# Performance work log

Hardware: AMD Instinct MI355X
Metric: run time of the kernel (lower is better)

Reference implementation:

```python
import jax, jax.numpy as jnp
import numpy as np
import math

NUM_HEADS = 16
HIDDEN = 1024
HEAD_DIM = HIDDEN // NUM_HEADS
MAX_POS = 512
BUCKET = 256
SCALE = 1.0 / math.sqrt(3.0 * HEAD_DIM)


def _make_log_bucket_position(rel_pos):
    # rel_pos: int32 [S, S]
    mid = BUCKET // 2
    rp = rel_pos.astype(jnp.float32)
    sign = jnp.sign(rp)
    abs_pos = jnp.where((rel_pos < mid) & (rel_pos > -mid), float(mid - 1), jnp.abs(rp))
    log_pos = jnp.ceil(jnp.log(abs_pos / mid) * (mid - 1) / math.log((MAX_POS - 1) / mid)) + mid
    bucket_pos = jnp.where(abs_pos <= mid, rp, log_pos * sign)
    return bucket_pos.astype(jnp.int32)


def _get_rel_pos(num_positions):
    ids = jnp.arange(num_positions, dtype=jnp.int32)
    rel_pos = ids[:, None] - ids[None, :]  # [S, S]
    return _make_log_bucket_position(rel_pos)


def setup_inputs() -> dict:
    key = jax.random.key(0)
    ks = jax.random.split(key, 10)
    B, S = 8, 512
    s_in = 1.0 / math.sqrt(HIDDEN)
    inputs = jax.random.normal(ks[0], (B, S, HIDDEN), dtype=jnp.float32)
    rel_embeddings = jax.random.normal(ks[1], (B, 2 * BUCKET, HIDDEN), dtype=jnp.float32)
    Wq = jax.random.normal(ks[2], (HIDDEN, NUM_HEADS, HEAD_DIM), dtype=jnp.float32) * s_in
    Wk = jax.random.normal(ks[3], (HIDDEN, NUM_HEADS, HEAD_DIM), dtype=jnp.float32) * s_in
    Wv = jax.random.normal(ks[4], (HIDDEN, NUM_HEADS, HEAD_DIM), dtype=jnp.float32) * s_in
    bq = jnp.zeros((NUM_HEADS, HEAD_DIM), dtype=jnp.float32)
    bk = jnp.zeros((NUM_HEADS, HEAD_DIM), dtype=jnp.float32)
    bv = jnp.zeros((NUM_HEADS, HEAD_DIM), dtype=jnp.float32)
    Wo = jax.random.normal(ks[5], (HIDDEN, HIDDEN), dtype=jnp.float32) * s_in
    bo = jnp.zeros((HIDDEN,), dtype=jnp.float32)
    return {"inputs": inputs, "rel_embeddings": rel_embeddings,
            "Wq": Wq, "bq": bq, "Wk": Wk, "bk": bk, "Wv": Wv, "bv": bv,
            "Wo": Wo, "bo": bo}


def reference(inputs, rel_embeddings, Wq, bq, Wk, bk, Wv, bv, Wo, bo):
    B, S, _ = inputs.shape
    # projections: [B,S,H,D]
    query = jnp.einsum('bsc,chd->bshd', inputs, Wq) + bq
    key = jnp.einsum('bsc,chd->bshd', inputs, Wk) + bk
    value = jnp.einsum('bsc,chd->bshd', inputs, Wv) + bv

    # content-content scores: [B,H,S_q,S_k]
    scores = jnp.einsum('bkhd,bqhd->bhqk', key, query) * SCALE

    # relative position projections on rel_embeddings [B,P,hidden], P=2*BUCKET
    pos_query = jnp.einsum('bpc,chd->bphd', rel_embeddings, Wq) + bq
    pos_key = jnp.einsum('bpc,chd->bphd', rel_embeddings, Wk) + bk

    rel_pos = _get_rel_pos(S)  # [S,S] int32
    span = BUCKET

    # c2p: query vs pos_key -> [B,H,S,P], gather along last axis
    c2p = jnp.einsum('bphd,bqhd->bhqp', pos_key, query)
    c2p_pos = jnp.clip(rel_pos + span, 0, 2 * span - 1)  # [S,S]
    c2p_idx = jnp.broadcast_to(c2p_pos[None, None], (B, NUM_HEADS, S, S))
    c2p = jnp.take_along_axis(c2p, c2p_idx, axis=3) * SCALE

    # p2c: key vs pos_query -> [B,H,S,P], gather then transpose
    p2c = jnp.einsum('bphd,bkhd->bhkp', pos_query, key)
    p2c_pos = jnp.clip(-rel_pos + span, 0, 2 * span - 1)
    p2c_idx = jnp.broadcast_to(p2c_pos[None, None], (B, NUM_HEADS, S, S))
    p2c = jnp.take_along_axis(p2c, p2c_idx, axis=3)
    p2c = jnp.swapaxes(p2c, 2, 3) * SCALE

    scores = scores + c2p + p2c
    probs = jax.nn.softmax(scores.astype(jnp.float32), axis=-1).astype(inputs.dtype)

    # attend: [B,S,H,D] -> [B,S,hidden]
    attn_out = jnp.einsum('bhqk,bkhd->bqhd', probs, value)
    attn_out = attn_out.reshape(B, S, HIDDEN)
    return jnp.einsum('bsc,cd->bsd', attn_out, Wo) + bo
```

## Files before the change

kernel.cpp:

```cpp
#include <hip/hip_runtime.h>

#define NUM_HEADS 16
#define HEAD_DIM  64
#define HIDDEN    1024
#define SEQ       512
#define BATCH     8
#define NBH       128
#define POSN      512
#define SCALE_F   0.07216878364870323f

typedef __attribute__((ext_vector_type(8))) short  short8;
typedef __attribute__((ext_vector_type(4))) short  short4_t;
typedef __attribute__((ext_vector_type(4))) float  floatx4;

#define GLDS16(gsrc, ldst) \
    __builtin_amdgcn_global_load_lds((const __attribute__((address_space(1))) void*)(gsrc), \
                                     (__attribute__((address_space(3))) void*)(ldst), 16, 0, 0)

__device__ __forceinline__ float bits2f(short s) {
    union { unsigned u; float f; } x;
    x.u = ((unsigned)(unsigned short)s) << 16;
    return x.f;
}
__device__ __forceinline__ short f2bits(float f) {
    union { float f; unsigned u; } x;
    x.f = f;
    unsigned r = x.u + 0x7fffu + ((x.u >> 16) & 1u);
    return (short)(r >> 16);
}

__global__ __launch_bounds__(256)
void prep_all(const float* __restrict__ a, const float* __restrict__ b,
              short* __restrict__ oa, short* __restrict__ ob,
              const float* __restrict__ w0, const float* __restrict__ w1,
              const float* __restrict__ w2, const float* __restrict__ w3,
              short* __restrict__ o0, short* __restrict__ o1,
              short* __restrict__ o2, short* __restrict__ o3,
              int* __restrict__ ftab)
{
    __shared__ float tile[64][65];
    const int bid = blockIdx.x, t = threadIdx.x;

    if (bid < 4096) {
        const int idx = bid * 256 + t;
        floatx4 va = ((const floatx4*)a)[idx];
        floatx4 vb = ((const floatx4*)b)[idx];
        short4_t ra, rb;
#pragma unroll
        for (int i = 0; i < 4; i++) { ra[i] = f2bits(va[i]); rb[i] = f2bits(vb[i]); }
        ((short4_t*)oa)[idx] = ra;
        ((short4_t*)ob)[idx] = rb;
        return;
    }
    if (bid < 5120) {
        const int r = bid - 4096;
        const int z = r >> 8, rem = r & 255;
        const float* src = (z == 0) ? w0 : (z == 1) ? w1 : (z == 2) ? w2 : w3;
        short*       dst = (z == 0) ? o0 : (z == 1) ? o1 : (z == 2) ? o2 : o3;
        const int c0 = (rem & 15) * 64, n0 = (rem >> 4) * 64;
#pragma unroll
        for (int j = 0; j < 16; j++) {
            const int e = t + j * 256;
            tile[e >> 6][e & 63] = src[(long)(c0 + (e >> 6)) * 1024 + n0 + (e & 63)];
        }
        __syncthreads();
#pragma unroll
        for (int j = 0; j < 16; j++) {
            const int e = t + j * 256;
            dst[(long)(n0 + (e >> 6)) * 1024 + c0 + (e & 63)] = f2bits(tile[e & 63][e >> 6]);
        }
        return;
    }
    const int i = (bid - 5120) * 256 + t;
    if (i >= 1023) return;
    const int delta = i - 511;
    const float Cf = (float)log(511.0 / 128.0);
    float absp = (delta < 128 && delta > -128) ? 127.0f : fabsf((float)delta);
    float bucket;
    if (absp <= 128.0f) {
        bucket = (float)delta;
    } else {
        float lp = ceilf((logf(absp * (1.0f / 128.0f)) * 127.0f) / Cf) + 128.0f;
        bucket = (delta > 0) ? lp : -lp;
    }
    int bi = (int)bucket + 256;
    bi = min(max(bi, 0), 511);
    ftab[i] = bi;
}

template<int MODE>
__global__ __launch_bounds__(256)
void gemm_nt(const short* __restrict__ A, long aBatch, int lda,
             const short* __restrict__ BT, long bBatch, int ldb,
             void* __restrict__ O0, void* __restrict__ O1, void* __restrict__ O2,
             long oBatch, int ldo,
             const float* __restrict__ b0, const float* __restrict__ b1,
             const float* __restrict__ b2, int Kd,
             const short* __restrict__ A2,
             void* __restrict__ O3, void* __restrict__ O4)
{
    __shared__ __align__(16) short As[2][128 * 64];
    __shared__ __align__(16) short Bs[2][128 * 64];

    int m0, n0, yy = 0;
    bool z1 = false;
    const int z = blockIdx.z;
    if (MODE == 6) {
        const int lin = blockIdx.x + (blockIdx.y << 5);
        const int swz = (lin & 7) * 160 + (lin >> 3);
        m0 = (swz & 31) * 128;
        yy = swz >> 5;
        z1 = (yy >= 24);
        n0 = (z1 ? (yy - 24) : yy) * 128;
    } else {
        m0 = blockIdx.x * 128;
        n0 = blockIdx.y * 128;
    }

    const short* Ab;
    const short* Bb;
    if (MODE == 6) {
        Ab = z1 ? A2 : A;
        Bb = BT;
    } else {
        Ab = A + (long)z * aBatch;
        Bb = BT + (long)z * bBatch;
    }

    const int t = threadIdx.x;
    const int l = t & 63, w = t >> 6;
    const int wm = w >> 1, wn = w & 1;
    const int lr = l & 15, lg = l >> 4;

    floatx4 acc[4][4];
#pragma unroll
    for (int i = 0; i < 4; i++)
#pragma unroll
        for (int j = 0; j < 4; j++) acc[i][j] = (floatx4){0.f, 0.f, 0.f, 0.f};

#pragma unroll
    for (int j = 0; j < 4; j++) {
        const int c = (w * 4 + j) * 64 + l;
        const int row = c >> 3, pc = c & 7;
        const int cc = pc ^ (row & 7);
        GLDS16(Ab + (long)(m0 + row) * lda + cc * 8, As[0] + c * 8);
        GLDS16(Bb + (long)(n0 + row) * ldb + cc * 8, Bs[0] + c * 8);
    }
    __syncthreads();

    int cur = 0;
    for (int k0 = 0; k0 < Kd; k0 += 64, cur ^= 1) {
        if (k0 + 64 < Kd) {
            const int kn = k0 + 64;
#pragma unroll
            for (int j = 0; j < 4; j++) {
                const int c = (w * 4 + j) * 64 + l;
                const int row = c >> 3, pc = c & 7;
                const int cc = pc ^ (row & 7);
                GLDS16(Ab + (long)(m0 + row) * lda + kn + cc * 8, As[cur ^ 1] + c * 8);
                GLDS16(Bb + (long)(n0 + row) * ldb + kn + cc * 8, Bs[cur ^ 1] + c * 8);
            }
        }
#pragma unroll
        for (int ks = 0; ks < 2; ks++) {
            short8 af[4], bfr[4];
#pragma unroll
            for (int i = 0; i < 4; i++) {
                const int mr = wm * 64 + i * 16 + lr;
                af[i] = *(const short8*)((char*)As[cur] + mr * 128 + (((ks * 4 + lg) ^ (mr & 7)) * 16));
                const int nr = wn * 64 + i * 16 + lr;
                bfr[i] = *(const short8*)((char*)Bs[cur] + nr * 128 + (((ks * 4 + lg) ^ (nr & 7)) * 16));
            }
#pragma unroll
            for (int i = 0; i < 4; i++)
#pragma unroll
                for (int j = 0; j < 4; j++)
                    acc[i][j] = __builtin_amdgcn_mfma_f32_16x16x32_bf16(af[i], bfr[j], acc[i][j], 0, 0, 0);
        }
        __syncthreads();
    }

    if (MODE == 6 && !z1 && yy >= 16) {
        short* tp = &As[0][0];
#pragma unroll
        for (int i = 0; i < 4; i++)
#pragma unroll
            for (int j = 0; j < 4; j++)
#pragma unroll
                for (int e = 0; e < 4; e++) {
                    const int ml  = wm * 64 + i * 16 + lg * 4 + e;
                    const int ngl = wn * 64 + j * 16 + lr;
                    const float v = acc[i][j][e] + b2[(n0 & 1023) + ngl];
                    tp[ngl * 128 + (ml ^ ((ngl & 7) << 4))] = f2bits(v);
                }
        __syncthreads();
        const int b = m0 >> 9, s0 = m0 & 511;
        const int hb = (n0 & 1023) >> 6;
        short* dst = (short*)O2;
#pragma unroll
        for (int j = 0; j < 8; j++) {
            const int task = t + j * 256;
            const int r = task >> 4, c = task & 15;
            short8 v8 = *(const short8*)(tp + r * 128 + ((c * 8) ^ ((r & 7) << 4)));
            const int h = hb + (r >> 6), d = r & 63;
            *(short8*)(dst + ((long)((b * NUM_HEADS + h) * HEAD_DIM + d)) * SEQ + s0 + c * 8) = v8;
        }
        return;
    }

#pragma unroll
    for (int i = 0; i < 4; i++) {
#pragma unroll
        for (int j = 0; j < 4; j++) {
#pragma unroll
            for (int e = 0; e < 4; e++) {
                const int mg = m0 + wm * 64 + i * 16 + lg * 4 + e;
                const int ng = n0 + wn * 64 + j * 16 + lr;
                float v = acc[i][j][e];
                if (MODE == 1) {
                    ((short*)O0)[(long)z * oBatch + (long)mg * ldo + ng] = f2bits(v);
                } else if (MODE == 2) {
                    ((float*)O0)[(long)mg * ldo + ng] = v + b0[ng];
                } else if (MODE == 6) {
                    const int hh = ng & 1023, mat = ng >> 10;
                    const int h = hh >> 6, d = hh & 63;
                    const int b = mg >> 9, s = mg & 511;
                    v += (mat == 0 ? b0 : b1)[hh];
                    short* dst;
                    if (z1) dst = (short*)(mat == 0 ? O3 : O4);
                    else    dst = (short*)(mat == 0 ? O0 : O1);
                    dst[((long)(b * NUM_HEADS + h) * SEQ + s) * HEAD_DIM + d] = f2bits(v);
                }
            }
        }
    }
}

template<int MODE>
__global__ __launch_bounds__(256)
void gemm_nt3(const short* __restrict__ A, long aBatch, int lda,
              const short* __restrict__ BT, long bBatch, int ldb,
              void* __restrict__ O0, long oBatch, int ldo,
              const float* __restrict__ b0, int Kd)
{
    __shared__ __align__(16) short LB[24576];

    const int z = blockIdx.z;
    const int m0 = blockIdx.x * 128, n0 = blockIdx.y * 128;
    const short* Ab = A + (long)z * aBatch;
    const short* Bb = BT + (long)z * bBatch;

    const int t = threadIdx.x;
    const int l = t & 63, w = t >> 6;
    const int wm = w >> 1, wn = w & 1;
    const int lr = l & 15, lg = l >> 4;

    const int c0c = t, c1c = t + 256;
    const int r0 = c0c >> 2, cc0 = (c0c & 3) ^ ((r0 >> 1) & 3);
    const int r1 = c1c >> 2, cc1 = (c1c & 3) ^ ((r1 >> 1) & 3);

    floatx4 acc[4][4];
#pragma unroll
    for (int i = 0; i < 4; i++)
#pragma unroll
        for (int j = 0; j < 4; j++) acc[i][j] = (floatx4){0.f, 0.f, 0.f, 0.f};

    const int niter = Kd >> 5;

    {
        GLDS16(Ab + (long)(m0 + r0) * lda + cc0 * 8, LB + c0c * 8);
        GLDS16(Ab + (long)(m0 + r1) * lda + cc1 * 8, LB + c1c * 8);
        GLDS16(Bb + (long)(n0 + r0) * ldb + cc0 * 8, LB + 12288 + c0c * 8);
        GLDS16(Bb + (long)(n0 + r1) * ldb + cc1 * 8, LB + 12288 + c1c * 8);
        GLDS16(Ab + (long)(m0 + r0) * lda + 32 + cc0 * 8, LB + 4096 + c0c * 8);
        GLDS16(Ab + (long)(m0 + r1) * lda + 32 + cc1 * 8, LB + 4096 + c1c * 8);
        GLDS16(Bb + (long)(n0 + r0) * ldb + 32 + cc0 * 8, LB + 12288 + 4096 + c0c * 8);
        GLDS16(Bb + (long)(n0 + r1) * ldb + 32 + cc1 * 8, LB + 12288 + 4096 + c1c * 8);
    }

    int cbase = 0;
    int ibase = 8192;
    for (int i = 0; i < niter; i++) {
        __builtin_amdgcn_sched_barrier(0);
        if (i + 1 < niter) { asm volatile("s_waitcnt vmcnt(4)" ::: "memory"); }
        else               { asm volatile("s_waitcnt vmcnt(0)" ::: "memory"); }
        __builtin_amdgcn_s_barrier();
        __builtin_amdgcn_sched_barrier(0);
        if (i + 2 < niter) {
            const int kn = (i + 2) << 5;
            GLDS16(Ab + (long)(m0 + r0) * lda + kn + cc0 * 8, LB + ibase + c0c * 8);
            GLDS16(Ab + (long)(m0 + r1) * lda + kn + cc1 * 8, LB + ibase + c1c * 8);
            GLDS16(Bb + (long)(n0 + r0) * ldb + kn + cc0 * 8, LB + 12288 + ibase + c0c * 8);
            GLDS16(Bb + (long)(n0 + r1) * ldb + kn + cc1 * 8, LB + 12288 + ibase + c1c * 8);
        }
        const short* Asb = LB + cbase;
        const short* Bsb = LB + 12288 + cbase;
        short8 af[4], bfr[4];
#pragma unroll
        for (int i4 = 0; i4 < 4; i4++) {
            const int mr = wm * 64 + i4 * 16 + lr;
            af[i4] = *(const short8*)((const char*)Asb + mr * 64 + ((lg ^ ((mr >> 1) & 3)) * 16));
            const int nr = wn * 64 + i4 * 16 + lr;
            bfr[i4] = *(const short8*)((const char*)Bsb + nr * 64 + ((lg ^ ((nr >> 1) & 3)) * 16));
        }
#pragma unroll
        for (int i4 = 0; i4 < 4; i4++)
#pragma unroll
            for (int j4 = 0; j4 < 4; j4++)
                acc[i4][j4] = __builtin_amdgcn_mfma_f32_16x16x32_bf16(af[i4], bfr[j4], acc[i4][j4], 0, 0, 0);
        cbase += 4096; if (cbase == 12288) cbase = 0;
        ibase += 4096; if (ibase == 12288) ibase = 0;
    }

#pragma unroll
    for (int i = 0; i < 4; i++) {
#pragma unroll
        for (int j = 0; j < 4; j++) {
#pragma unroll
            for (int e = 0; e < 4; e++) {
                const int mg = m0 + wm * 64 + i * 16 + lg * 4 + e;
                const int ng = n0 + wn * 64 + j * 16 + lr;
                float v = acc[i][j][e];
                if (MODE == 1) {
                    ((short*)O0)[(long)z * oBatch + (long)mg * ldo + ng] = f2bits(v);
                } else {
                    ((float*)O0)[(long)mg * ldo + ng] = v + b0[ng];
                }
            }
        }
    }
}

__global__ __launch_bounds__(512, 2)
void p2c_fused(const short* __restrict__ posQ, const short* __restrict__ K,
               const short* __restrict__ c2pf, const int* __restrict__ ftab,
               short* __restrict__ Bias)
{
    __shared__ __align__(16) short As[512 * 64];
    __shared__ __align__(16) short Bs[64 * 64];
    __shared__ short ft[1024];
    const int lin = blockIdx.x;
    const int swz = (lin & 7) * 128 + (lin >> 3);
    const int bh = swz >> 3, ko = swz & 7;
    const int k0 = ko * 64;
    const int t = threadIdx.x, l = t & 63, w = t >> 6;
    const int lr = l & 15, lg = l >> 4;
    const short* Ab = posQ + (long)bh * SEQ * HEAD_DIM;
    const short* Kb = K + (long)bh * SEQ * HEAD_DIM;
    const short* c2pb = c2pf + (long)bh * SEQ * POSN;

    for (int i = t; i < 1024; i += 512) ft[i] = (short)((i < 1023) ? ftab[i] : 0);

#pragma unroll
    for (int j = 0; j < 8; j++) {
        const int c = j * 512 + t;
        const int row = c >> 3, pc = c & 7;
        const int cc = pc ^ (row & 7);
        GLDS16(Ab + (long)row * HEAD_DIM + cc * 8, As + c * 8);
    }
    {
        const int c = t;
        const int row = c >> 3, pc = c & 7;
        const int cc = pc ^ (row & 7);
        GLDS16(Kb + (long)(k0 + row) * HEAD_DIM + cc * 8, Bs + c * 8);
    }
    __syncthreads();

    floatx4 acc[4][4];
#pragma unroll
    for (int i = 0; i < 4; i++)
#pragma unroll
        for (int j = 0; j < 4; j++) acc[i][j] = (floatx4){0.f, 0.f, 0.f, 0.f};
#pragma unroll
    for (int ks = 0; ks < 2; ks++) {
        short8 af[4], bfr[4];
#pragma unroll
        for (int i = 0; i < 4; i++) {
            const int mr = w * 64 + i * 16 + lr;
            af[i] = *(const short8*)((char*)As + mr * 128 + (((ks * 4 + lg) ^ (mr & 7)) * 16));
            const int nr = i * 16 + lr;
            bfr[i] = *(const short8*)((char*)Bs + nr * 128 + (((ks * 4 + lg) ^ (nr & 7)) * 16));
        }
#pragma unroll
        for (int i = 0; i < 4; i++)
#pragma unroll
            for (int j = 0; j < 4; j++)
                acc[i][j] = __builtin_amdgcn_mfma_f32_16x16x32_bf16(af[i], bfr[j], acc[i][j], 0, 0, 0);
    }
    __syncthreads();

#pragma unroll
    for (int i = 0; i < 4; i++)
#pragma unroll
        for (int j = 0; j < 4; j++)
#pragma unroll
            for (int e = 0; e < 4; e++) {
                const int p = w * 64 + i * 16 + lg * 4 + e;
                const int kk = j * 16 + lr;
                As[p * 64 + (kk ^ (lg << 4))] = f2bits(acc[i][j][e]);
            }
    __syncthreads();

    short* Bb = Bias + (long)bh * SEQ * SEQ;
#pragma unroll
    for (int j = 0; j < 8; j++) {
        const int task = j * 512 + t;
        const int qt = task >> 8;
        const int kl = (task >> 2) & 63;
        const int rc = task & 3;
        const int k  = k0 + kl;
        short8 v;
#pragma unroll
        for (int i = 0; i < 8; i++) {
            const int q  = qt * 32 + rc * 8 + i;
            const int fk = (int)ft[q - k + 511];
            const float sv = bits2f(As[fk * 64 + (kl ^ (((fk >> 2) & 3) << 4))]);
            const float cv = bits2f(c2pb[(long)q * POSN + fk]);
            v[i] = f2bits(sv + cv);
        }
        short* Bq = Bb + qt * 16384;
        const int mt  = rc >> 1;
        const int lg0 = (rc * 2) & 3;
        const int pb  = (((mt * 4 + (k >> 7)) * 8 + ((k >> 4) & 7)) * 64
                         + (lg0 * 16 + (k & 15))) * 4;
        *(short4_t*)(Bq + pb)      = (short4_t){v[0], v[1], v[2], v[3]};
        *(short4_t*)(Bq + pb + 64) = (short4_t){v[4], v[5], v[6], v[7]};
    }
}

__global__ __launch_bounds__(256, 4)
void attn_fused(const short* __restrict__ Q, const short* __restrict__ K,
                const short* __restrict__ Vt, const short* __restrict__ Bias,
                short* __restrict__ attnO)
{
    __shared__ __align__(16) short PS[32 * 512];
    __shared__ float red[4][32];

    const int lin  = blockIdx.x;
    const int lin2 = (lin & 7) * 256 + (lin >> 3);
    const int bh = lin2 >> 4, qt = lin2 & 15;
    const int q0 = qt * 32;
    const int t = threadIdx.x, l = t & 63, w = t >> 6;
    const int lr = l & 15, lg = l >> 4;
    const long pbase = (long)bh * SEQ * HEAD_DIM;
    const short* Qb  = Q  + pbase;
    const short* Kb  = K  + pbase;
    const short* Vtb = Vt + pbase;
    const short* Bb  = Bias + ((long)bh * 16 + qt) * (512 * 32);

    short4_t bfrag[2][8];
#pragma unroll
    for (int mt = 0; mt < 2; mt++)
#pragma unroll
        for (int nt = 0; nt < 8; nt++)
            bfrag[mt][nt] = *(const short4_t*)(Bb + ((((mt * 4 + w) * 8 + nt) * 64 + l) << 2));

    short8 aq[2][2];
#pragma unroll
    for (int mt = 0; mt < 2; mt++)
#pragma unroll
        for (int ks = 0; ks < 2; ks++)
            aq[mt][ks] = *(const short8*)(Qb + (q0 + mt * 16 + lr) * 64 + ks * 32 + lg * 8);

    floatx4 acc[2][8];
#pragma unroll
    for (int mt = 0; mt < 2; mt++)
#pragma unroll
        for (int nt = 0; nt < 8; nt++) acc[mt][nt] = (floatx4){0.f, 0.f, 0.f, 0.f};

    __builtin_amdgcn_s_setprio(1);
#pragma unroll
    for (int nt = 0; nt < 8; nt++) {
        const int kr = w * 128 + nt * 16 + lr;
        short8 kb0 = *(const short8*)(Kb + kr * 64 + lg * 8);
        short8 kb1 = *(const short8*)(Kb + kr * 64 + 32 + lg * 8);
#pragma unroll
        for (int mt = 0; mt < 2; mt++) {
            acc[mt][nt] = __builtin_amdgcn_mfma_f32_16x16x32_bf16(aq[mt][0], kb0, acc[mt][nt], 0, 0, 0);
            acc[mt][nt] = __builtin_amdgcn_mfma_f32_16x16x32_bf16(aq[mt][1], kb1, acc[mt][nt], 0, 0, 0);
        }
    }
    __builtin_amdgcn_s_setprio(0);

#pragma unroll
    for (int mt = 0; mt < 2; mt++)
#pragma unroll
        for (int e = 0; e < 4; e++) {
            const int r = mt * 16 + lg * 4 + e;
            float s = 0.f;
#pragma unroll
            for (int nt = 0; nt < 8; nt++) {
                float p = __expf((acc[mt][nt][e] + bits2f(bfrag[mt][nt][e])) * SCALE_F);
                acc[mt][nt][e] = p;
                s += p;
            }
            s += __shfl_xor(s, 1); s += __shfl_xor(s, 2);
            s += __shfl_xor(s, 4); s += __shfl_xor(s, 8);
            red[w][r] = s;
#pragma unroll
            for (int nt = 0; nt < 8; nt++) {
                const int kcol = w * 128 + nt * 16 + lr;
                int byte = r * 1024 + kcol * 2;
                byte ^= (r & 7) << 4;
                *(short*)((char*)PS + byte) = f2bits(acc[mt][nt][e]);
            }
        }
    __syncthreads();

    floatx4 accO[2];
    accO[0] = (floatx4){0.f, 0.f, 0.f, 0.f};
    accO[1] = (floatx4){0.f, 0.f, 0.f, 0.f};
    __builtin_amdgcn_s_setprio(1);
#pragma unroll
    for (int ks = 0; ks < 16; ks++) {
        short8 vb = *(const short8*)(Vtb + (long)(w * 16 + lr) * SEQ + ks * 32 + lg * 8);
#pragma unroll
        for (int mt = 0; mt < 2; mt++) {
            const int qr = mt * 16 + lr;
            int byte = qr * 1024 + (ks * 32 + lg * 8) * 2;
            byte ^= (qr & 7) << 4;
            short8 pa = *(const short8*)((char*)PS + byte);
            accO[mt] = __builtin_amdgcn_mfma_f32_16x16x32_bf16(pa, vb, accO[mt], 0, 0, 0);
        }
    }
    __builtin_amdgcn_s_setprio(0);

    const int b = bh >> 4, h = bh & 15;
#pragma unroll
    for (int mt = 0; mt < 2; mt++)
#pragma unroll
        for (int e = 0; e < 4; e++) {
            const int r = mt * 16 + lg * 4 + e;
            const float rs = red[0][r] + red[1][r] + red[2][r] + red[3][r];
            const float v = accO[mt][e] / rs;
            attnO[((long)(b * SEQ + q0 + r)) * HIDDEN + h * HEAD_DIM + w * 16 + lr] = f2bits(v);
        }
}

extern "C" void kernel_launch(void* const* d_in, const int* in_sizes, int n_in,
                              void* d_out, int out_size, void* d_ws, size_t ws_size,
                              hipStream_t stream)
{
    const float* inputs = (const float*)d_in[0];
    const float* rel    = (const float*)d_in[1];
    const float* Wq     = (const float*)d_in[2];
    const float* bq     = (const float*)d_in[3];
    const float* Wk     = (const float*)d_in[4];
    const float* bk     = (const float*)d_in[5];
    const float* Wv     = (const float*)d_in[6];
    const float* bv     = (const float*)d_in[7];
    const float* Wo     = (const float*)d_in[8];
    const float* bo     = (const float*)d_in[9];
    float* out = (float*)d_out;

    char* ws = (char*)d_ws;
    size_t off = 0;
    auto alloc = [&](size_t bytes) -> char* {
        char* p = ws + off;
        off += (bytes + 255) & ~(size_t)255;
        return p;
    };
    short* inA   = (short*)alloc(4194304ull * 2);
    short* inRel = (short*)alloc(4194304ull * 2);
    short* WqT   = (short*)alloc(1048576ull * 2);
    short* WkT   = (short*)alloc(1048576ull * 2);
    short* WvT   = (short*)alloc(1048576ull * 2);
    short* WoT   = (short*)alloc(1048576ull * 2);
    short* Qw    = (short*)alloc(4194304ull * 2);
    short* Kw    = (short*)alloc(4194304ull * 2);
    short* Vtw   = (short*)alloc(4194304ull * 2);
    short* posQw = (short*)alloc(4194304ull * 2);
    short* posKw = (short*)alloc(4194304ull * 2);
    short* c2pW  = (short*)alloc(33554432ull * 2);
    short* BW    = (short*)alloc(33554432ull * 2);
    short* attnW = (short*)alloc(4194304ull * 2);
    int*   ftabW = (int*)alloc(4096);

    prep_all<<<5124, 256, 0, stream>>>(inputs, rel, inA, inRel,
                                       Wq, Wk, Wv, Wo, WqT, WkT, WvT, WoT, ftabW);

    gemm_nt<6><<<dim3(32, 40), 256, 0, stream>>>(inA, 0, 1024, WqT, 0, 1024,
                                                 Qw, Kw, Vtw, 0, 0, bq, bk, bv, 1024,
                                                 inRel, posQw, posKw);

    gemm_nt3<1><<<dim3(4, 4, 128), 256, 0, stream>>>(Qw, 32768, 64, posKw, 32768, 64,
                                                     c2pW, 262144, 512, nullptr, 64);

    p2c_fused<<<1024, 512, 0, stream>>>(posQw, Kw, c2pW, ftabW, BW);

    attn_fused<<<2048, 256, 0, stream>>>(Qw, Kw, Vtw, BW, attnW);

    gemm_nt3<2><<<dim3(32, 8), 256, 0, stream>>>(attnW, 0, 1024, WoT, 0, 1024,
                                                 out, 0, 1024, bo, 1024);
}
```

Before: 188.6 us.

## Deepen GEMM global-to-LDS prefetch with explicit vmcnt waits and barriers

Restructures the GEMM main loop so that two K-tiles are in flight. The next-next tile is issued after compute finishes on the current buffer, and each iteration waits with s_waitcnt vmcnt(8) rather than a full drain. The goal is to hide global-load latency behind MFMA work instead of stalling at __syncthreads for every load. The code depends on the exact count of outstanding vm ops (8 per tile) and uses sched_barriers to pin the order, which is fragile if other memory ops get interleaved.

```diff
diff --git a/kernel.cpp b/kernel.cpp
--- a/kernel.cpp
+++ b/kernel.cpp
@@ -138,6 +138,8 @@
 #pragma unroll
         for (int j = 0; j < 4; j++) acc[i][j] = (floatx4){0.f, 0.f, 0.f, 0.f};
 
+    const int niter = Kd >> 6;
+
 #pragma unroll
     for (int j = 0; j < 4; j++) {
         const int c = (w * 4 + j) * 64 + l;
@@ -146,39 +148,56 @@
         GLDS16(Ab + (long)(m0 + row) * lda + cc * 8, As[0] + c * 8);
         GLDS16(Bb + (long)(n0 + row) * ldb + cc * 8, Bs[0] + c * 8);
     }
-    __syncthreads();
+    if (niter > 1) {
+#pragma unroll
+        for (int j = 0; j < 4; j++) {
+            const int c = (w * 4 + j) * 64 + l;
+            const int row = c >> 3, pc = c & 7;
+            const int cc = pc ^ (row & 7);
+            GLDS16(Ab + (long)(m0 + row) * lda + 64 + cc * 8, As[1] + c * 8);
+            GLDS16(Bb + (long)(n0 + row) * ldb + 64 + cc * 8, Bs[1] + c * 8);
+        }
+    }
 
     int cur = 0;
-    for (int k0 = 0; k0 < Kd; k0 += 64, cur ^= 1) {
-        if (k0 + 64 < Kd) {
-            const int kn = k0 + 64;
+    for (int i = 0; i < niter; i++, cur ^= 1) {
+        __builtin_amdgcn_sched_barrier(0);
+        if (i + 1 < niter) { asm volatile("s_waitcnt vmcnt(8)" ::: "memory"); }
+        else               { asm volatile("s_waitcnt vmcnt(0)" ::: "memory"); }
+        __builtin_amdgcn_s_barrier();
+        __builtin_amdgcn_sched_barrier(0);
+#pragma unroll
+        for (int ks = 0; ks < 2; ks++) {
+            short8 af[4], bfr[4];
+#pragma unroll
+            for (int i4 = 0; i4 < 4; i4++) {
+                const int mr = wm * 64 + i4 * 16 + lr;
+                af[i4] = *(const short8*)((char*)As[cur] + mr * 128 + (((ks * 4 + lg) ^ (mr & 7)) * 16));
+                const int nr = wn * 64 + i4 * 16 + lr;
+                bfr[i4] = *(const short8*)((char*)Bs[cur] + nr * 128 + (((ks * 4 + lg) ^ (nr & 7)) * 16));
+            }
+#pragma unroll
+            for (int i4 = 0; i4 < 4; i4++)
+#pragma unroll
+                for (int j4 = 0; j4 < 4; j4++)
+                    acc[i4][j4] = __builtin_amdgcn_mfma_f32_16x16x32_bf16(af[i4], bfr[j4], acc[i4][j4], 0, 0, 0);
+        }
+        __builtin_amdgcn_sched_barrier(0);
+        __builtin_amdgcn_s_barrier();
+        __builtin_amdgcn_sched_barrier(0);
+        if (i + 2 < niter) {
+            const int kn = (i + 2) << 6;
 #pragma unroll
             for (int j = 0; j < 4; j++) {
                 const int c = (w * 4 + j) * 64 + l;
                 const int row = c >> 3, pc = c & 7;
                 const int cc = pc ^ (row & 7);
-                GLDS16(Ab + (long)(m0 + row) * lda + kn + cc * 8, As[cur ^ 1] + c * 8);
-                GLDS16(Bb + (long)(n0 + row) * ldb + kn + cc * 8, Bs[cur ^ 1] + c * 8);
+                GLDS16(Ab + (long)(m0 + row) * lda + kn + cc * 8, As[cur] + c * 8);
+                GLDS16(Bb + (long)(n0 + row) * ldb + kn + cc * 8, Bs[cur] + c * 8);
             }
         }
-#pragma unroll
-        for (int ks = 0; ks < 2; ks++) {
-            short8 af[4], bfr[4];
-#pragma unroll
-            for (int i = 0; i < 4; i++) {
-                const int mr = wm * 64 + i * 16 + lr;
-                af[i] = *(const short8*)((char*)As[cur] + mr * 128 + (((ks * 4 + lg) ^ (mr & 7)) * 16));
-                const int nr = wn * 64 + i * 16 + lr;
-                bfr[i] = *(const short8*)((char*)Bs[cur] + nr * 128 + (((ks * 4 + lg) ^ (nr & 7)) * 16));
-            }
-#pragma unroll
-            for (int i = 0; i < 4; i++)
-#pragma unroll
-                for (int j = 0; j < 4; j++)
-                    acc[i][j] = __builtin_amdgcn_mfma_f32_16x16x32_bf16(af[i], bfr[j], acc[i][j], 0, 0, 0);
-        }
-        __syncthreads();
-    }
+    }
+    __syncthreads();
 
     if (MODE == 6 && !z1 && yy >= 16) {
         short* tp = &As[0][0];
```

New measurement: 193.7 us. 2.7% more time.
